# Kernel tuning notes

Hardware: AMD Instinct MI355X
Metric: run time of the kernel (lower is better)

Reference implementation:

```python
import jax, jax.numpy as jnp
import numpy as np

N, E, D, H = 40000, 640000, 128, 8
DH = D // H  # out_feats per head
EPS = 1e-5


def _layernorm(x, g, b):
    mu = jnp.mean(x, axis=-1, keepdims=True)
    var = jnp.mean(jnp.square(x - mu), axis=-1, keepdims=True)
    return (x - mu) * jax.lax.rsqrt(var + EPS) * g + b


def setup_inputs() -> dict:
    key = jax.random.key(0)
    ks = jax.random.split(key, 12)
    s = 0.02
    return {
        "feat": jax.random.normal(ks[0], (N, D), dtype=jnp.float32),
        "src": jax.random.randint(ks[1], (E,), 0, N, dtype=jnp.int32),
        "dst": jax.random.randint(ks[2], (E,), 0, N, dtype=jnp.int32),
        "Wq": jax.random.normal(ks[3], (D, D), dtype=jnp.float32) * s,
        "Wk": jax.random.normal(ks[4], (D, D), dtype=jnp.float32) * s,
        "Wv": jax.random.normal(ks[5], (D, D), dtype=jnp.float32) * s,
        "ln1_g": jnp.ones((D,), jnp.float32),
        "ln1_b": jnp.zeros((D,), jnp.float32),
        "ln2_g": jnp.ones((D,), jnp.float32),
        "ln2_b": jnp.zeros((D,), jnp.float32),
        "W1": jax.random.normal(ks[6], (D, 4 * D), dtype=jnp.float32) * s,
        "b1": jnp.zeros((4 * D,), jnp.float32),
        "prelu_w": jnp.full((4 * D,), 0.25, jnp.float32),
        "W2": jax.random.normal(ks[7], (4 * D, D), dtype=jnp.float32) * s,
        "b2": jnp.zeros((D,), jnp.float32),
    }


def reference(feat, src, dst, Wq, Wk, Wv, ln1_g, ln1_b, ln2_g, ln2_b,
              W1, b1, prelu_w, W2, b2):
    n = feat.shape[0]
    feat_c = jax.lax.stop_gradient(feat)  # .clone().detach()
    q = (feat @ Wq).reshape(n, H, DH)
    k = (feat_c @ Wk).reshape(n, H, DH)
    v = (feat_c @ Wv).reshape(n, H, DH)

    # u_dot_v: per-edge, per-head dot product of k at src and q at dst
    scores = jnp.einsum('ehd,ehd->eh', k[src], q[dst]) / np.float32(np.sqrt(DH * H))

    # edge_softmax: softmax over incoming edges of each destination node
    smax = jax.ops.segment_max(scores, dst, num_segments=n)  # [N,H]
    sexp = jnp.exp(scores - smax[dst])
    ssum = jax.ops.segment_sum(sexp, dst, num_segments=n)
    a = sexp / ssum[dst]  # [E,H]  (attn_drop is eval no-op)

    # u_mul_e + sum: weighted scatter-aggregate of v[src] into dst
    msgs = v[src] * a[:, :, None]  # [E,H,DH]
    ft2 = jax.ops.segment_sum(msgs, dst, num_segments=n).reshape(n, D)

    rst = _layernorm(ft2 + feat, ln1_g, ln1_b)
    h = rst @ W1 + b1
    h = jnp.where(h >= 0, h, prelu_w * h)  # PReLU, per-channel
    ffn = h @ W2 + b2  # ffn_drop is eval no-op
    return _layernorm(rst + ffn, ln2_g, ln2_b)
```

## Files before the change

kernel.cpp:

```cpp
#include <hip/hip_runtime.h>
#include <hip/hip_bf16.h>
#include <math.h>

#define DIM 128
#define NHEAD 8
#define DHEAD 16
#define HID 512
#define LN_EPS 1e-5f
#define QSCALE 0.12751879104863297f

typedef __bf16 bf16x8 __attribute__((ext_vector_type(8)));
typedef float f32x4 __attribute__((ext_vector_type(4)));
typedef float f32x2 __attribute__((ext_vector_type(2)));
typedef _Float16 f16x2 __attribute__((ext_vector_type(2)));

__device__ inline float bf2f(unsigned int bits16) {
    return __uint_as_float(bits16 << 16);
}
__device__ inline unsigned short f2bf(float f) {
    unsigned int u = __float_as_uint(f);
    unsigned int r = u + 0x7fff + ((u >> 16) & 1);
    return (unsigned short)(r >> 16);
}
__device__ inline unsigned short f2h(float f) {
    _Float16 h = (_Float16)f;
    return __builtin_bit_cast(unsigned short, h);
}
__device__ inline float h2f(unsigned short h) {
    return (float)__builtin_bit_cast(_Float16, h);
}
__device__ inline unsigned short pk_fp8(float a, float b) {
    int r = __builtin_amdgcn_cvt_pk_fp8_f32(a, b, 0, false);
    return (unsigned short)(r & 0xffff);
}
__device__ inline f32x2 unpk_fp8_lo(unsigned int w) {
    return __builtin_amdgcn_cvt_pk_f32_fp8((int)w, false);
}
__device__ inline float fexp2(float x) { return __builtin_amdgcn_exp2f(x); }

__device__ inline void gload_lds16(const void* g, void* l) {
    __builtin_amdgcn_global_load_lds(
        (const __attribute__((address_space(1))) unsigned int*)g,
        (__attribute__((address_space(3))) unsigned int*)l, 16, 0, 0);
}

__global__ __launch_bounds__(256) void prep_count_kernel(
        int* counts, int Nn,
        const float* __restrict__ feat, unsigned short* __restrict__ featb,
        const float* __restrict__ Wq, const float* __restrict__ Wk, const float* __restrict__ Wv,
        unsigned short* __restrict__ Wqkvt,
        const float* __restrict__ W1, unsigned short* __restrict__ W1t,
        const float* __restrict__ W2, unsigned short* __restrict__ W2t,
        const int* __restrict__ dst, int E, int fb, int wb) {
    int blk = blockIdx.x, t = threadIdx.x;
    if (blk < fb) {
        int i = blk * 256 + t;
        if (i < Nn * 32) {
            float4 v = *(const float4*)(feat + (size_t)i * 4);
            ushort4 o;
            o.x = f2bf(v.x); o.y = f2bf(v.y); o.z = f2bf(v.z); o.w = f2bf(v.w);
            *(ushort4*)(featb + (size_t)i * 4) = o;
        }
    } else if (blk < wb) {
        int b2_ = blk - fb;
        if (b2_ < 192) {
            int sec = b2_ >> 6;
            const float* W = sec == 0 ? Wq : (sec == 1 ? Wk : Wv);
            int o = (b2_ & 63) * 256 + t;
            int oc = o >> 7, orow = o & 127;
            Wqkvt[sec * 16384 + o] = f2bf(W[(size_t)orow * 128 + oc]);
        } else if (b2_ < 448) {
            int o = (b2_ - 192) * 256 + t;
            int oc = o >> 7, orow = o & 127;
            W1t[o] = f2bf(W1[(size_t)orow * 512 + oc]);
        } else {
            int o = (b2_ - 448) * 256 + t;
            int oc = o >> 9, orow = o & 511;
            W2t[o] = f2bf(W2[(size_t)orow * 128 + oc]);
        }
    } else {
        int e0 = (blk - wb) * 1024 + t * 4;
        if (e0 + 3 < E) {
            int4 d = *(const int4*)(dst + e0);
            atomicAdd(&counts[d.x], 1);
            atomicAdd(&counts[d.y], 1);
            atomicAdd(&counts[d.z], 1);
            atomicAdd(&counts[d.w], 1);
        } else {
            for (int e = e0; e < E; ++e) atomicAdd(&counts[dst[e]], 1);
        }
    }
}


__global__ __launch_bounds__(256) void scanA_kernel(const int* __restrict__ counts, int* bsum, int Nn) {
    int blk = blockIdx.x, t = threadIdx.x;
    int i = blk * 1024 + t * 4;
    int s = 0;
    if (i < Nn) { int4 x = *(const int4*)(counts + i); s = x.x + x.y + x.z + x.w; }
#pragma unroll
    for (int off = 1; off < 64; off <<= 1) s += __shfl_xor(s, off, 64);
    __shared__ int wt[4];
    if ((t & 63) == 0) wt[t >> 6] = s;
    __syncthreads();
    if (t == 0) bsum[blk] = wt[0] + wt[1] + wt[2] + wt[3];
}

__global__ __launch_bounds__(256) void scanC_kernel(int* counts, const int* __restrict__ bsum,
                                                    int* offsets, int Nn, int NCH) {
    int blk = blockIdx.x, t = threadIdx.x, lane = t & 63, wv = t >> 6;
    __shared__ int wt[4];
    __shared__ int base_s;
    if (wv == 0) {
        int v = (lane < NCH) ? bsum[lane] : 0;
        int s = v;
#pragma unroll
        for (int off = 1; off < 64; off <<= 1) {
            int u = __shfl_up(s, off, 64);
            if (lane >= off) s += u;
        }
        int basev = (blk > 0) ? __shfl(s, blk - 1, 64) : 0;
        int tot = __shfl(s, NCH - 1, 64);
        if (lane == 0) {
            base_s = basev;
            if (blk == 0) offsets[Nn] = tot;
        }
    }
    int i = blk * 1024 + t * 4;
    int4 x = make_int4(0, 0, 0, 0);
    if (i < Nn) x = *(const int4*)(counts + i);
    int ts = x.x + x.y + x.z + x.w;
    int s = ts;
#pragma unroll
    for (int off = 1; off < 64; off <<= 1) {
        int u = __shfl_up(s, off, 64);
        if (lane >= off) s += u;
    }
    if (lane == 63) wt[wv] = s;
    __syncthreads();
    int woff = 0;
    for (int wi = 0; wi < wv; ++wi) woff += wt[wi];
    int excl = base_s + woff + (s - ts);
    if (i < Nn) {
        int o0 = excl, o1 = o0 + x.x, o2 = o1 + x.y, o3 = o2 + x.z;
        *(int4*)(offsets + i) = make_int4(o0, o1, o2, o3);
        *(int4*)(counts + i) = make_int4(o0, o1, o2, o3);
    }
}

#define QST 136
__global__ __launch_bounds__(256) void fill_qkv_kernel(
        const int* __restrict__ dst, const int* __restrict__ src,
        int* cursor, int* srcs, int E, int cb,
        const unsigned short* __restrict__ A, const unsigned short* __restrict__ Bt,
        unsigned short* __restrict__ qb, unsigned char* __restrict__ kv8) {
    int blk = blockIdx.x, t = threadIdx.x;
    if (blk < cb) {
        int e0 = blk * 1024 + t * 4;
        if (e0 + 3 < E) {
            int4 d = *(const int4*)(dst + e0);
            int4 sv = *(const int4*)(src + e0);
            srcs[atomicAdd(&cursor[d.x], 1)] = sv.x;
            srcs[atomicAdd(&cursor[d.y], 1)] = sv.y;
            srcs[atomicAdd(&cursor[d.z], 1)] = sv.z;
            srcs[atomicAdd(&cursor[d.w], 1)] = sv.w;
        } else {
            for (int e = e0; e < E; ++e) srcs[atomicAdd(&cursor[dst[e]], 1)] = src[e];
        }
        return;
    }
    __shared__ unsigned short smem[128 * QST];
    unsigned short* As = smem;
    unsigned short* Bs = smem + 4096;
    int q = blk - cb;
    int region = q % 3;
    int m0 = (q / 3) * 128;
    int wave = t >> 6, lane = t & 63;
    int wr = wave >> 1, wc = wave & 1;
    int lrow = lane & 15, kq = lane >> 4;
    int n0 = region * 128;
    int srow = t >> 2, scol8 = (t & 3) * 8;

    f32x4 acc[4][4] = {};
    for (int k0 = 0; k0 < 128; k0 += 32) {
        gload_lds16(A + (size_t)(m0 + srow) * 128 + k0 + scol8,      As + t * 8);
        gload_lds16(A + (size_t)(m0 + 64 + srow) * 128 + k0 + scol8, As + 2048 + t * 8);
        gload_lds16(Bt + (size_t)(n0 + srow) * 128 + k0 + scol8,      Bs + t * 8);
        gload_lds16(Bt + (size_t)(n0 + 64 + srow) * 128 + k0 + scol8, Bs + 2048 + t * 8);
        __syncthreads();
        bf16x8 af[4], bfr[4];
#pragma unroll
        for (int mi = 0; mi < 4; ++mi)
            af[mi] = *(const bf16x8*)(&As[(wr * 64 + mi * 16 + lrow) * 32 + kq * 8]);
#pragma unroll
        for (int ni = 0; ni < 4; ++ni)
            bfr[ni] = *(const bf16x8*)(&Bs[(wc * 64 + ni * 16 + lrow) * 32 + kq * 8]);
#pragma unroll
        for (int mi = 0; mi < 4; ++mi)
#pragma unroll
            for (int ni = 0; ni < 4; ++ni)
                acc[mi][ni] = __builtin_amdgcn_mfma_f32_16x16x32_bf16(af[mi], bfr[ni], acc[mi][ni], 0, 0, 0);
        __syncthreads();
    }

    float scale = (region == 0) ? QSCALE : 1.f;
#pragma unroll
    for (int ni = 0; ni < 4; ++ni) {
        int col = wc * 64 + ni * 16 + lrow;
#pragma unroll
        for (int mi = 0; mi < 4; ++mi) {
#pragma unroll
            for (int r = 0; r < 4; ++r) {
                int row = wr * 64 + mi * 16 + kq * 4 + r;
                smem[row * QST + col] = f2h(acc[mi][ni][r] * scale);
            }
        }
    }
    __syncthreads();
    if (region == 0) {
        unsigned short* outp = qb + (size_t)m0 * 128;
#pragma unroll
        for (int i = 0; i < 8; ++i) {
            int chunk = i * 256 + t;
            int row = chunk >> 4, c16 = chunk & 15;
            *(float4*)(outp + (size_t)chunk * 8) = *(const float4*)(smem + row * QST + c16 * 8);
        }
    } else {
        int half = region - 1;
#pragma unroll
        for (int i = 0; i < 4; ++i) {
            int chunk = i * 256 + t;
            int row = chunk >> 3, seg = chunk & 7;
            const unsigned short* sp = smem + row * QST + seg * 16;
            unsigned int ow[4];
#pragma unroll
            for (int j = 0; j < 4; ++j) {
                unsigned int lo = pk_fp8(h2f(sp[4 * j]), h2f(sp[4 * j + 1]));
                unsigned int hi = pk_fp8(h2f(sp[4 * j + 2]), h2f(sp[4 * j + 3]));
                ow[j] = lo | (hi << 16);
            }
            *(uint4*)(kv8 + (size_t)(m0 + row) * 256 + half * 128 + seg * 16) =
                make_uint4(ow[0], ow[1], ow[2], ow[3]);
        }
    }
}

__global__ __launch_bounds__(256) void agg_ln1_kernel(
        const unsigned short* __restrict__ qb, const unsigned short* __restrict__ kvu,
        const float* __restrict__ feat,
        const int* __restrict__ srcs, const int* __restrict__ offsets,
        const float* __restrict__ g, const float* __restrict__ b,
        unsigned short* __restrict__ rstb, int n) {
    int node = blockIdx.x * 4 + (threadIdx.x >> 6);
    int lane = threadIdx.x & 63;
    if (node >= n) return;

    unsigned int qw = ((const unsigned int*)qb)[(size_t)node * 64 + lane];
    f16x2 qp = __builtin_bit_cast(f16x2, qw);
    float q0 = (float)qp.x, q1 = (float)qp.y;

    int beg = offsets[node], end = offsets[node + 1];
    float l = 0.f, a0 = 0.f, a1 = 0.f;

    for (int idx = beg; idx < end; idx += 8) {
        int sa[8];
#pragma unroll
        for (int i = 0; i < 8; ++i) {
            int ii = idx + i;
            sa[i] = (ii < end) ? srcs[ii] : -1;
        }
        unsigned int kw[8], vw[8];
#pragma unroll
        for (int i = 0; i < 8; ++i) {
            int s = sa[i] < 0 ? 0 : sa[i];
            kw[i] = kvu[(size_t)s * 128 + lane];
        }
#pragma unroll
        for (int i = 0; i < 8; ++i) {
            int s = sa[i] < 0 ? 0 : sa[i];
            vw[i] = kvu[(size_t)s * 128 + 64 + lane];
        }
        float sc[8];
#pragma unroll
        for (int i = 0; i < 8; ++i) {
            f32x2 kk = unpk_fp8_lo(kw[i]);
            float p = fmaf(kk.x, q0, kk.y * q1);
            p += __shfl_xor(p, 1, 8);
            p += __shfl_xor(p, 2, 8);
            p += __shfl_xor(p, 4, 8);
            p = fminf(fmaxf(p, -30.f), 30.f);
            sc[i] = (sa[i] < 0) ? -1000.f : p;
        }
#pragma unroll
        for (int i = 0; i < 8; ++i) {
            float ww = fexp2(sc[i]);
            f32x2 vv = unpk_fp8_lo(vw[i]);
            l += ww;
            a0 = fmaf(vv.x, ww, a0);
            a1 = fmaf(vv.y, ww, a1);
        }
    }

    float inv = (l > 0.f) ? 1.f / l : 0.f;
    float2 fv = *(const float2*)(feat + (size_t)node * DIM + 2 * lane);
    float x0 = a0 * inv + fv.x;
    float x1 = a1 * inv + fv.y;

    float s1 = x0 + x1;
    float s2 = x0 * x0 + x1 * x1;
#pragma unroll
    for (int off = 1; off < 64; off <<= 1) {
        s1 += __shfl_xor(s1, off, 64);
        s2 += __shfl_xor(s2, off, 64);
    }
    float mean = s1 * (1.f / DIM);
    float var = s2 * (1.f / DIM) - mean * mean;
    float rinv = rsqrtf(var + LN_EPS);
    float g0 = g[2 * lane], g1 = g[2 * lane + 1];
    float b0 = b[2 * lane], b1 = b[2 * lane + 1];
    float o0 = (x0 - mean) * rinv * g0 + b0;
    float o1 = (x1 - mean) * rinv * g1 + b1;
    unsigned int packed = (unsigned int)f2bf(o0) | ((unsigned int)f2bf(o1) << 16);
    ((unsigned int*)rstb)[(size_t)node * 64 + lane] = packed;
}

__global__ __launch_bounds__(256) void ffn1_gemm(
        const unsigned short* __restrict__ A, const unsigned short* __restrict__ Bt,
        unsigned short* __restrict__ hid,
        const float* __restrict__ b1, const float* __restrict__ prelu) {
    __shared__ unsigned short smem[128 * QST];
    unsigned short* As = smem;
    unsigned short* Bs = smem + 4096;
    int t = threadIdx.x;
    int wave = t >> 6, lane = t & 63;
    int wr = wave >> 1, wc = wave & 1;
    int lrow = lane & 15, kq = lane >> 4;
    int m0 = blockIdx.y * 128;
    int n0 = blockIdx.x * 128;
    int srow = t >> 2, scol8 = (t & 3) * 8;

    f32x4 acc[4][4] = {};
    for (int k0 = 0; k0 < 128; k0 += 32) {
        gload_lds16(A + (size_t)(m0 + srow) * 128 + k0 + scol8,      As + t * 8);
        gload_lds16(A + (size_t)(m0 + 64 + srow) * 128 + k0 + scol8, As + 2048 + t * 8);
        gload_lds16(Bt + (size_t)(n0 + srow) * 128 + k0 + scol8,      Bs + t * 8);
        gload_lds16(Bt + (size_t)(n0 + 64 + srow) * 128 + k0 + scol8, Bs + 2048 + t * 8);
        __syncthreads();
        bf16x8 af[4], bfr[4];
#pragma unroll
        for (int mi = 0; mi < 4; ++mi)
            af[mi] = *(const bf16x8*)(&As[(wr * 64 + mi * 16 + lrow) * 32 + kq * 8]);
#pragma unroll
        for (int ni = 0; ni < 4; ++ni)
            bfr[ni] = *(const bf16x8*)(&Bs[(wc * 64 + ni * 16 + lrow) * 32 + kq * 8]);
#pragma unroll
        for (int mi = 0; mi < 4; ++mi)
#pragma unroll
            for (int ni = 0; ni < 4; ++ni)
                acc[mi][ni] = __builtin_amdgcn_mfma_f32_16x16x32_bf16(af[mi], bfr[ni], acc[mi][ni], 0, 0, 0);
        __syncthreads();
    }

#pragma unroll
    for (int ni = 0; ni < 4; ++ni) {
        int col = wc * 64 + ni * 16 + lrow;
        int cg = n0 + col;
        float biv = b1[cg], pwv = prelu[cg];
#pragma unroll
        for (int mi = 0; mi < 4; ++mi) {
#pragma unroll
            for (int r = 0; r < 4; ++r) {
                int row = wr * 64 + mi * 16 + kq * 4 + r;
                float v = acc[mi][ni][r] + biv;
                v = v >= 0.f ? v : pwv * v;
                smem[row * QST + col] = f2bf(v);
            }
        }
    }
    __syncthreads();
#pragma unroll
    for (int i = 0; i < 8; ++i) {
        int chunk = i * 256 + t;
        int row = chunk >> 4, c16 = chunk & 15;
        *(float4*)(hid + (size_t)(m0 + row) * 512 + n0 + c16 * 8) =
            *(const float4*)(smem + row * QST + c16 * 8);
    }
}

__global__ __launch_bounds__(256) void ffn2_ln2_kernel(
        const unsigned short* __restrict__ hid, const unsigned short* __restrict__ W2t,
        const unsigned short* __restrict__ rstb,
        const float* __restrict__ b2, const float* __restrict__ g, const float* __restrict__ bb,
        float* __restrict__ out, int Nn) {
    __shared__ unsigned short As[64 * 32];
    __shared__ unsigned short Bs[128 * 32];
    __shared__ float redS[64][4];
    __shared__ float redQ[64][4];
    int t = threadIdx.x;
    int wave = t >> 6, lane = t & 63;
    int lrow = lane & 15, kq = lane >> 4;
    int m0 = blockIdx.x * 64;
    int srow = t >> 2, scol8 = (t & 3) * 8;

    f32x4 acc[4][2] = {};
    for (int k0 = 0; k0 < 512; k0 += 32) {
        gload_lds16(hid + (size_t)(m0 + srow) * 512 + k0 + scol8, As + t * 8);
        gload_lds16(W2t + (size_t)srow * 512 + k0 + scol8,        Bs + t * 8);
        gload_lds16(W2t + (size_t)(64 + srow) * 512 + k0 + scol8, Bs + 2048 + t * 8);
        __syncthreads();
        bf16x8 af[4], bfr[2];
#pragma unroll
        for (int mi = 0; mi < 4; ++mi)
            af[mi] = *(const bf16x8*)(&As[(mi * 16 + lrow) * 32 + kq * 8]);
#pragma unroll
        for (int ni = 0; ni < 2; ++ni)
            bfr[ni] = *(const bf16x8*)(&Bs[(wave * 32 + ni * 16 + lrow) * 32 + kq * 8]);
#pragma unroll
        for (int mi = 0; mi < 4; ++mi)
#pragma unroll
            for (int ni = 0; ni < 2; ++ni)
                acc[mi][ni] = __builtin_amdgcn_mfma_f32_16x16x32_bf16(af[mi], bfr[ni], acc[mi][ni], 0, 0, 0);
        __syncthreads();
    }

    float b2v[2], gv[2], bv[2];
    int cols[2];
#pragma unroll
    for (int ni = 0; ni < 2; ++ni) {
        cols[ni] = wave * 32 + ni * 16 + lrow;
        b2v[ni] = b2[cols[ni]]; gv[ni] = g[cols[ni]]; bv[ni] = bb[cols[ni]];
    }
#pragma unroll
    for (int mi = 0; mi < 4; ++mi) {
#pragma unroll
        for (int r = 0; r < 4; ++r) {
            int rloc = mi * 16 + kq * 4 + r;
            int row = m0 + rloc;
            float ps = 0.f, pq = 0.f;
#pragma unroll
            for (int ni = 0; ni < 2; ++ni) {
                float rsv = bf2f(rstb[(size_t)row * 128 + cols[ni]]);
                float v = acc[mi][ni][r] + b2v[ni] + rsv;
                acc[mi][ni][r] = v;
                ps += v; pq += v * v;
            }
#pragma unroll
            for (int off = 1; off < 16; off <<= 1) {
                ps += __shfl_xor(ps, off, 16);
                pq += __shfl_xor(pq, off, 16);
            }
            if (lrow == 0) { redS[rloc][wave] = ps; redQ[rloc][wave] = pq; }
        }
    }
    __syncthreads();
#pragma unroll
    for (int mi = 0; mi < 4; ++mi) {
#pragma unroll
        for (int r = 0; r < 4; ++r) {
            int rloc = mi * 16 + kq * 4 + r;
            int row = m0 + rloc;
            float s1 = redS[rloc][0] + redS[rloc][1] + redS[rloc][2] + redS[rloc][3];
            float sq = redQ[rloc][0] + redQ[rloc][1] + redQ[rloc][2] + redQ[rloc][3];
            float mean = s1 * (1.f / DIM);
            float var = sq * (1.f / DIM) - mean * mean;
            float rs = rsqrtf(var + LN_EPS);
            if (row < Nn) {
#pragma unroll
                for (int ni = 0; ni < 2; ++ni)
                    out[(size_t)row * 128 + cols[ni]] =
                        (acc[mi][ni][r] - mean) * rs * gv[ni] + bv[ni];
            }
        }
    }
}


extern "C" void kernel_launch(void* const* d_in, const int* in_sizes, int n_in,
                              void* d_out, int out_size, void* d_ws, size_t ws_size,
                              hipStream_t stream) {
    const float* feat   = (const float*)d_in[0];
    const int*   src    = (const int*)d_in[1];
    const int*   dst    = (const int*)d_in[2];
    const float* Wq     = (const float*)d_in[3];
    const float* Wk     = (const float*)d_in[4];
    const float* Wv     = (const float*)d_in[5];
    const float* ln1_g  = (const float*)d_in[6];
    const float* ln1_b  = (const float*)d_in[7];
    const float* ln2_g  = (const float*)d_in[8];
    const float* ln2_b  = (const float*)d_in[9];
    const float* W1     = (const float*)d_in[10];
    const float* b1     = (const float*)d_in[11];
    const float* prelu  = (const float*)d_in[12];
    const float* W2     = (const float*)d_in[13];
    const float* b2     = (const float*)d_in[14];
    float* out = (float*)d_out;

    const int Nn = in_sizes[0] / DIM;
    const int E  = in_sizes[1];
    const int MP = (Nn + 127) & ~127;

    char* w = (char*)d_ws;
    unsigned short* qb   = (unsigned short*)w; w += (size_t)MP * DIM * 2;
    unsigned char*  kv8  = (unsigned char*)w;  w += (size_t)MP * 256;
    unsigned short* rstb = (unsigned short*)w; w += (size_t)MP * DIM * 2;
    unsigned short* featb= (unsigned short*)w; w += (size_t)MP * DIM * 2;
    unsigned short* hid  = (unsigned short*)w; w += (size_t)MP * HID * 2;
    unsigned short* Wqkvt= (unsigned short*)w; w += 3 * DIM * DIM * 2;
    unsigned short* W1t  = (unsigned short*)w; w += (size_t)HID * DIM * 2;
    unsigned short* W2t  = (unsigned short*)w; w += (size_t)DIM * HID * 2;
    int* counts  = (int*)w;  w += (size_t)Nn * 4;
    int* offsets = (int*)w;  w += (size_t)(Nn + 4) * 4;
    int* bsum    = (int*)w;  w += 64 * 4;
    int* srcs    = (int*)w;

    const int NCH = (Nn + 1023) / 1024;
    const int FB  = Nn / 8;
    const int WB  = FB + 704;
    const int CB  = (E + 1023) / 1024;

    hipMemsetAsync(counts, 0, (size_t)Nn * 4, stream);

    prep_count_kernel<<<WB + CB, 256, 0, stream>>>(
        counts, Nn, feat, featb, Wq, Wk, Wv, Wqkvt, W1, W1t, W2, W2t, dst, E, FB, WB);

    scanA_kernel<<<NCH, 256, 0, stream>>>(counts, bsum, Nn);
    scanC_kernel<<<NCH, 256, 0, stream>>>(counts, bsum, offsets, Nn, NCH);

    fill_qkv_kernel<<<CB + 3 * (MP / 128), 256, 0, stream>>>(
        dst, src, counts, srcs, E, CB, featb, Wqkvt, qb, kv8);

    agg_ln1_kernel<<<(Nn + 3) / 4, 256, 0, stream>>>(qb, (const unsigned short*)kv8, feat,
                                                     srcs, offsets, ln1_g, ln1_b, rstb, Nn);

    {
        dim3 grid(4, MP / 128);
        ffn1_gemm<<<grid, 256, 0, stream>>>(rstb, W1t, hid, b1, prelu);
    }

    ffn2_ln2_kernel<<<MP / 64, 256, 0, stream>>>(hid, W2t, rstb, b2, ln2_g, ln2_b, out, Nn);
}
```

Before: 259.5 us.

## Remap aggregation lanes to edge-by-head with 16-byte loads and transpose reduction

The aggregation kernel now gives each lane one (edge, head) pair, so every lane holds a full 16-dim head slice of q and loads whole 16-byte k and v chunks per edge. The old layout needed shuffle reductions for every edge's score. The per-edge partial accumulators are combined at the end with a butterfly transpose-reduce across the eight edge groups. This cuts shuffle traffic and widens memory accesses, at the cost of more registers (16 accumulators plus 16 q values) and possible lane waste when a node has few incoming edges.

```diff
diff --git a/kernel.cpp b/kernel.cpp
--- a/kernel.cpp
+++ b/kernel.cpp
@@ -36,12 +36,42 @@
 __device__ inline f32x2 unpk_fp8_lo(unsigned int w) {
     return __builtin_amdgcn_cvt_pk_f32_fp8((int)w, false);
 }
+__device__ inline f32x2 unpk_fp8_hi(unsigned int w) {
+    return __builtin_amdgcn_cvt_pk_f32_fp8((int)w, true);
+}
 __device__ inline float fexp2(float x) { return __builtin_amdgcn_exp2f(x); }
 
 __device__ inline void gload_lds16(const void* g, void* l) {
     __builtin_amdgcn_global_load_lds(
         (const __attribute__((address_space(1))) unsigned int*)g,
         (__attribute__((address_space(3))) unsigned int*)l, 16, 0, 0);
+}
+
+__device__ __forceinline__ float dot16_fp8(uint4 w, const float (&q)[16]) {
+    f32x2 a0 = unpk_fp8_lo(w.x), b0 = unpk_fp8_hi(w.x);
+    f32x2 a1 = unpk_fp8_lo(w.y), b1 = unpk_fp8_hi(w.y);
+    f32x2 a2 = unpk_fp8_lo(w.z), b2 = unpk_fp8_hi(w.z);
+    f32x2 a3 = unpk_fp8_lo(w.w), b3 = unpk_fp8_hi(w.w);
+    float t0 = fmaf(a0.x, q[0],  fmaf(a0.y, q[1],  fmaf(b0.x, q[2],  b0.y * q[3])));
+    float t1 = fmaf(a1.x, q[4],  fmaf(a1.y, q[5],  fmaf(b1.x, q[6],  b1.y * q[7])));
+    float t2 = fmaf(a2.x, q[8],  fmaf(a2.y, q[9],  fmaf(b2.x, q[10], b2.y * q[11])));
+    float t3 = fmaf(a3.x, q[12], fmaf(a3.y, q[13], fmaf(b3.x, q[14], b3.y * q[15])));
+    return (t0 + t1) + (t2 + t3);
+}
+
+__device__ __forceinline__ void pv16_fp8(uint4 w, float wt, float (&acc)[16]) {
+    f32x2 a0 = unpk_fp8_lo(w.x), b0 = unpk_fp8_hi(w.x);
+    f32x2 a1 = unpk_fp8_lo(w.y), b1 = unpk_fp8_hi(w.y);
+    f32x2 a2 = unpk_fp8_lo(w.z), b2 = unpk_fp8_hi(w.z);
+    f32x2 a3 = unpk_fp8_lo(w.w), b3 = unpk_fp8_hi(w.w);
+    acc[0]  = fmaf(a0.x, wt, acc[0]);  acc[1]  = fmaf(a0.y, wt, acc[1]);
+    acc[2]  = fmaf(b0.x, wt, acc[2]);  acc[3]  = fmaf(b0.y, wt, acc[3]);
+    acc[4]  = fmaf(a1.x, wt, acc[4]);  acc[5]  = fmaf(a1.y, wt, acc[5]);
+    acc[6]  = fmaf(b1.x, wt, acc[6]);  acc[7]  = fmaf(b1.y, wt, acc[7]);
+    acc[8]  = fmaf(a2.x, wt, acc[8]);  acc[9]  = fmaf(a2.y, wt, acc[9]);
+    acc[10] = fmaf(b2.x, wt, acc[10]); acc[11] = fmaf(b2.y, wt, acc[11]);
+    acc[12] = fmaf(a3.x, wt, acc[12]); acc[13] = fmaf(a3.y, wt, acc[13]);
+    acc[14] = fmaf(b3.x, wt, acc[14]); acc[15] = fmaf(b3.y, wt, acc[15]);
 }
 
 __global__ __launch_bounds__(256) void prep_count_kernel(
@@ -246,7 +276,7 @@
 }
 
 __global__ __launch_bounds__(256) void agg_ln1_kernel(
-        const unsigned short* __restrict__ qb, const unsigned short* __restrict__ kvu,
+        const unsigned short* __restrict__ qb, const unsigned char* __restrict__ kv8,
         const float* __restrict__ feat,
         const int* __restrict__ srcs, const int* __restrict__ offsets,
         const float* __restrict__ g, const float* __restrict__ b,
@@ -254,74 +284,109 @@
     int node = blockIdx.x * 4 + (threadIdx.x >> 6);
     int lane = threadIdx.x & 63;
     if (node >= n) return;
-
-    unsigned int qw = ((const unsigned int*)qb)[(size_t)node * 64 + lane];
-    f16x2 qp = __builtin_bit_cast(f16x2, qw);
-    float q0 = (float)qp.x, q1 = (float)qp.y;
+    int el = lane >> 3;
+    int h  = lane & 7;
+
+    const uint4* qp = (const uint4*)(qb + (size_t)node * 128 + h * 16);
+    uint4 qlo = qp[0], qhi = qp[1];
+    float qf[16];
+    {
+        unsigned int qw[8] = {qlo.x, qlo.y, qlo.z, qlo.w, qhi.x, qhi.y, qhi.z, qhi.w};
+#pragma unroll
+        for (int j = 0; j < 8; ++j) {
+            f16x2 p2 = __builtin_bit_cast(f16x2, qw[j]);
+            qf[2 * j]     = (float)p2.x;
+            qf[2 * j + 1] = (float)p2.y;
+        }
+    }
 
     int beg = offsets[node], end = offsets[node + 1];
-    float l = 0.f, a0 = 0.f, a1 = 0.f;
-
-    for (int idx = beg; idx < end; idx += 8) {
-        int sa[8];
-#pragma unroll
-        for (int i = 0; i < 8; ++i) {
-            int ii = idx + i;
-            sa[i] = (ii < end) ? srcs[ii] : -1;
-        }
-        unsigned int kw[8], vw[8];
-#pragma unroll
-        for (int i = 0; i < 8; ++i) {
-            int s = sa[i] < 0 ? 0 : sa[i];
-            kw[i] = kvu[(size_t)s * 128 + lane];
-        }
-#pragma unroll
-        for (int i = 0; i < 8; ++i) {
-            int s = sa[i] < 0 ? 0 : sa[i];
-            vw[i] = kvu[(size_t)s * 128 + 64 + lane];
-        }
-        float sc[8];
-#pragma unroll
-        for (int i = 0; i < 8; ++i) {
-            f32x2 kk = unpk_fp8_lo(kw[i]);
-            float p = fmaf(kk.x, q0, kk.y * q1);
-            p += __shfl_xor(p, 1, 8);
-            p += __shfl_xor(p, 2, 8);
-            p += __shfl_xor(p, 4, 8);
-            p = fminf(fmaxf(p, -30.f), 30.f);
-            sc[i] = (sa[i] < 0) ? -1000.f : p;
-        }
-#pragma unroll
-        for (int i = 0; i < 8; ++i) {
-            float ww = fexp2(sc[i]);
-            f32x2 vv = unpk_fp8_lo(vw[i]);
-            l += ww;
-            a0 = fmaf(vv.x, ww, a0);
-            a1 = fmaf(vv.y, ww, a1);
-        }
-    }
+    float l = 0.f;
+    float acc[16];
+#pragma unroll
+    for (int j = 0; j < 16; ++j) acc[j] = 0.f;
+
+    for (int idx = beg; idx < end; idx += 16) {
+        int e0i = idx + el, e1i = idx + 8 + el;
+        bool v0 = e0i < end, v1 = e1i < end;
+        int s0 = srcs[v0 ? e0i : beg];
+        int s1 = srcs[v1 ? e1i : beg];
+        const uint4* kp0 = (const uint4*)(kv8 + (size_t)s0 * 256 + h * 16);
+        const uint4* kp1 = (const uint4*)(kv8 + (size_t)s1 * 256 + h * 16);
+        uint4 kw0 = kp0[0];
+        uint4 vw0 = kp0[8];
+        uint4 kw1 = kp1[0];
+        uint4 vw1 = kp1[8];
+
+        float p0 = dot16_fp8(kw0, qf);
+        float p1 = dot16_fp8(kw1, qf);
+        float sc0 = v0 ? fminf(fmaxf(p0, -30.f), 30.f) : -1000.f;
+        float sc1 = v1 ? fminf(fmaxf(p1, -30.f), 30.f) : -1000.f;
+        float w0 = fexp2(sc0);
+        float w1 = fexp2(sc1);
+        l += w0 + w1;
+        pv16_fp8(vw0, w0, acc);
+        pv16_fp8(vw1, w1, acc);
+    }
+
+    l += __shfl_xor(l, 8, 64);
+    l += __shfl_xor(l, 16, 64);
+    l += __shfl_xor(l, 32, 64);
+
+    float r8[8];
+    {
+        bool b0 = (el & 1) != 0;
+#pragma unroll
+        for (int j = 0; j < 8; ++j) {
+            float send = b0 ? acc[j] : acc[j + 8];
+            float keep = b0 ? acc[j + 8] : acc[j];
+            r8[j] = keep + __shfl_xor(send, 8, 64);
+        }
+    }
+    float r4[4];
+    {
+        bool b1 = (el & 2) != 0;
+#pragma unroll
+        for (int j = 0; j < 4; ++j) {
+            float send = b1 ? r8[j] : r8[j + 4];
+            float keep = b1 ? r8[j + 4] : r8[j];
+            r4[j] = keep + __shfl_xor(send, 16, 64);
+        }
+    }
+    float r2[2];
+    {
+        bool b2 = (el & 4) != 0;
+#pragma unroll
+        for (int j = 0; j < 2; ++j) {
+            float send = b2 ? r4[j] : r4[j + 2];
+            float keep = b2 ? r4[j + 2] : r4[j];
+            r2[j] = keep + __shfl_xor(send, 32, 64);
+        }
+    }
+    int off = ((el & 1) << 3) | ((el & 2) << 1) | ((el & 4) >> 1);
+    int d0 = h * 16 + off;
 
     float inv = (l > 0.f) ? 1.f / l : 0.f;
-    float2 fv = *(const float2*)(feat + (size_t)node * DIM + 2 * lane);
-    float x0 = a0 * inv + fv.x;
-    float x1 = a1 * inv + fv.y;
+    float2 fv = *(const float2*)(feat + (size_t)node * DIM + d0);
+    float x0 = r2[0] * inv + fv.x;
+    float x1 = r2[1] * inv + fv.y;
 
     float s1 = x0 + x1;
     float s2 = x0 * x0 + x1 * x1;
 #pragma unroll
-    for (int off = 1; off < 64; off <<= 1) {
-        s1 += __shfl_xor(s1, off, 64);
-        s2 += __shfl_xor(s2, off, 64);
+    for (int off2 = 1; off2 < 64; off2 <<= 1) {
+        s1 += __shfl_xor(s1, off2, 64);
+        s2 += __shfl_xor(s2, off2, 64);
     }
     float mean = s1 * (1.f / DIM);
     float var = s2 * (1.f / DIM) - mean * mean;
     float rinv = rsqrtf(var + LN_EPS);
-    float g0 = g[2 * lane], g1 = g[2 * lane + 1];
-    float b0 = b[2 * lane], b1 = b[2 * lane + 1];
-    float o0 = (x0 - mean) * rinv * g0 + b0;
-    float o1 = (x1 - mean) * rinv * g1 + b1;
+    float2 gv = *(const float2*)(g + d0);
+    float2 bv = *(const float2*)(b + d0);
+    float o0 = (x0 - mean) * rinv * gv.x + bv.x;
+    float o1 = (x1 - mean) * rinv * gv.y + bv.y;
     unsigned int packed = (unsigned int)f2bf(o0) | ((unsigned int)f2bf(o1) << 16);
-    ((unsigned int*)rstb)[(size_t)node * 64 + lane] = packed;
+    ((unsigned int*)rstb)[(size_t)node * 64 + (d0 >> 1)] = packed;
 }
 
 __global__ __launch_bounds__(256) void ffn1_gemm(
@@ -529,7 +594,7 @@
     fill_qkv_kernel<<<CB + 3 * (MP / 128), 256, 0, stream>>>(
         dst, src, counts, srcs, E, CB, featb, Wqkvt, qb, kv8);
 
-    agg_ln1_kernel<<<(Nn + 3) / 4, 256, 0, stream>>>(qb, (const unsigned short*)kv8, feat,
+    agg_ln1_kernel<<<(Nn + 3) / 4, 256, 0, stream>>>(qb, kv8, feat,
                                                      srcs, offsets, ln1_g, ln1_b, rstb, Nn);
 
     {
```

New measurement: 259.1 us. About the same (-0.2%).
